# Performance work log

Hardware: AMD Instinct MI355X
Metric: run time of the kernel (lower is better)

The kernel has to match this reference:

```python
import jax, jax.numpy as jnp
import numpy as np

N, E = 50000, 600000
IN, PE, H, L, K = 112, 16, 128, 64, 4


def setup_inputs() -> dict:
    key = jax.random.key(0)
    ks = jax.random.split(key, 8)
    x = jax.random.normal(ks[0], (N, IN), jnp.float32)
    edge_index = jax.random.randint(ks[1], (2, E), 0, N, dtype=jnp.int64)
    lap_pe = jax.random.normal(ks[2], (N, PE), jnp.float32)
    edge_weight = jax.random.uniform(ks[3], (E,), jnp.float32)
    s = lambda k, shp, fan: jax.random.normal(k, shp, jnp.float32) / np.sqrt(fan).astype(np.float32)
    W1 = s(ks[4], (K, IN + PE, H), IN + PE)
    b1 = jnp.zeros((H,), jnp.float32)
    W2 = s(ks[5], (K, H, H), H)
    b2 = jnp.zeros((H,), jnp.float32)
    Wmu = s(ks[6], (H, L), H)
    bmu = jnp.zeros((L,), jnp.float32)
    Wlv = s(ks[7], (H, L), H)
    blv = jnp.zeros((L,), jnp.float32)
    return dict(x=x, edge_index=edge_index, lap_pe=lap_pe, edge_weight=edge_weight,
                W1=W1, b1=b1, W2=W2, b2=b2, Wmu=Wmu, bmu=bmu, Wlv=Wlv, blv=blv)


def _cheb_conv(h, src, dst, w, W, b):
    """PyG ChebConv with precomputed scaled-Laplacian edge weights w.
    T_0 = h ; T_1 = That h ; T_k = 2 That T_{k-1} - T_{k-2}; out = sum_k T_k W_k + b."""
    n = h.shape[0]
    prop = lambda t: jax.ops.segment_sum(w[:, None] * t[src], dst, num_segments=n)
    Tx0 = h
    out = Tx0 @ W[0]
    Tx1 = prop(Tx0)
    out = out + Tx1 @ W[1]
    for k in range(2, W.shape[0]):
        Tx2 = 2.0 * prop(Tx1) - Tx0
        out = out + Tx2 @ W[k]
        Tx0, Tx1 = Tx1, Tx2
    return out + b


def reference(x, edge_index, lap_pe, edge_weight, W1, b1, W2, b2, Wmu, bmu, Wlv, blv):
    n = x.shape[0]
    src, dst = edge_index[0], edge_index[1]
    # sym-normalized Laplacian, lambda_max=2 -> That = L_sym - I = -D^-1/2 A D^-1/2
    deg = jax.ops.segment_sum(edge_weight, src, num_segments=n)
    dis = jnp.where(deg > 0, jax.lax.rsqrt(jnp.maximum(deg, 1e-12)), 0.0)
    w = -dis[src] * edge_weight * dis[dst]
    h = jnp.concatenate([x, lap_pe], axis=1)  # [N, in+pe]
    h = jax.nn.relu(_cheb_conv(h, src, dst, w, W1, b1))
    h = jax.nn.relu(_cheb_conv(h, src, dst, w, W2, b2))
    mu = h @ Wmu + bmu
    logvar = h @ Wlv + blv
    return (mu, logvar)
```

## Files before the change

kernel.cpp:

```cpp
#include <hip/hip_runtime.h>


typedef __bf16 bf16x8 __attribute__((ext_vector_type(8)));
typedef float f32x4 __attribute__((ext_vector_type(4)));
typedef unsigned int uint32;
typedef unsigned short ushort16;

__device__ inline ushort16 f2bf(float f) {
    uint32 x = __float_as_uint(f);
    uint32 r = x + 0x7fffu + ((x >> 16) & 1u);
    return (ushort16)(r >> 16);
}
__device__ inline float bflo(uint32 v) { return __uint_as_float(v << 16); }
__device__ inline float bfhi(uint32 v) { return __uint_as_float(v & 0xffff0000u); }


__global__ void k_deg_cnt(const int* __restrict__ src, const int* __restrict__ dst,
                          const float* __restrict__ ew, float* __restrict__ deg,
                          int* __restrict__ cnt, int* __restrict__ pos,
                          int e0, int e1) {
    int e = e0 + blockIdx.x * blockDim.x + threadIdx.x;
    if (e >= e1) return;
    atomicAdd(&deg[src[e]], ew[e]);
    pos[e] = atomicAdd(&cnt[dst[e]], 1);
}

__global__ void k_scan_blk(const int* __restrict__ cnt, int* __restrict__ row_ptr,
                           int* __restrict__ blk_sums, int N) {
    __shared__ int wsum[4];
    const int tid = threadIdx.x;
    const int base = blockIdx.x * 1024 + tid * 4;
    int4 v = make_int4(0, 0, 0, 0);
    if (base + 3 < N) v = *(const int4*)&cnt[base];
    else {
        if (base + 0 < N) v.x = cnt[base + 0];
        if (base + 1 < N) v.y = cnt[base + 1];
        if (base + 2 < N) v.z = cnt[base + 2];
    }
    const int tsum = v.x + v.y + v.z + v.w;
    const int lane = tid & 63;
    const int wv = tid >> 6;
    int incl = tsum;
    #pragma unroll
    for (int off = 1; off < 64; off <<= 1) {
        int t = __shfl_up(incl, off);
        if (lane >= off) incl += t;
    }
    if (lane == 63) wsum[wv] = incl;
    __syncthreads();
    int woff = 0;
    #pragma unroll
    for (int w = 0; w < 4; ++w) if (w < wv) woff += wsum[w];
    const int excl = woff + incl - tsum;
    if (base + 0 < N) row_ptr[base + 0] = excl;
    if (base + 1 < N) row_ptr[base + 1] = excl + v.x;
    if (base + 2 < N) row_ptr[base + 2] = excl + v.x + v.y;
    if (base + 3 < N) row_ptr[base + 3] = excl + v.x + v.y + v.z;
    if (tid == 255) blk_sums[blockIdx.x] = woff + incl;
}

__global__ void k_scan_top(int* __restrict__ blk_sums, int* __restrict__ row_ptr,
                           int nblk, int N) {
    const int lane = threadIdx.x;
    int v = (lane < nblk) ? blk_sums[lane] : 0;
    int incl = v;
    #pragma unroll
    for (int off = 1; off < 64; off <<= 1) {
        int t = __shfl_up(incl, off);
        if (lane >= off) incl += t;
    }
    if (lane < nblk) blk_sums[lane] = incl - v;
    if (lane == 63) row_ptr[N] = incl;
}

__global__ void k_fix_dis(int* __restrict__ row_ptr, const int* __restrict__ blk_sums,
                          const float* __restrict__ deg, float* __restrict__ dis, int N) {
    int i = blockIdx.x * blockDim.x + threadIdx.x;
    if (i >= N) return;
    row_ptr[i] += blk_sums[i >> 10];
    float d = deg[i];
    dis[i] = d > 0.f ? rsqrtf(fmaxf(d, 1e-12f)) : 0.f;
}

__global__ void k_scatter(const int* __restrict__ src, const int* __restrict__ dst,
                          const float* __restrict__ ew, const float* __restrict__ dis,
                          const int* __restrict__ row_ptr, const int* __restrict__ pos,
                          int2* __restrict__ csr, int E) {
    int e = blockIdx.x * blockDim.x + threadIdx.x;
    if (e >= E) return;
    int s = src[e], d = dst[e];
    float wv = -dis[s] * ew[e] * dis[d];
    csr[row_ptr[d] + pos[e]] = make_int2(s, __float_as_int(wv));
}


__global__ void k_concat_bf16(const float* __restrict__ x, const float* __restrict__ pe,
                              uint32* __restrict__ h, int N) {
    int i4 = (blockIdx.x * blockDim.x + threadIdx.x) * 4;
    if (i4 >= N * 64) return;
    int node = i4 >> 6, p = i4 & 63;
    float4 fa, fb;
    if (p < 56) {
        const float* xp = &x[(size_t)node * 112 + p * 2];
        fa = *(const float4*)xp; fb = *(const float4*)(xp + 4);
    } else {
        const float* pp = &pe[(size_t)node * 16 + (p - 56) * 2];
        fa = *(const float4*)pp; fb = *(const float4*)(pp + 4);
    }
    int4 o;
    o.x = (uint32)f2bf(fa.x) | ((uint32)f2bf(fa.y) << 16);
    o.y = (uint32)f2bf(fa.z) | ((uint32)f2bf(fa.w) << 16);
    o.z = (uint32)f2bf(fb.x) | ((uint32)f2bf(fb.y) << 16);
    o.w = (uint32)f2bf(fb.z) | ((uint32)f2bf(fb.w) << 16);
    *(int4*)&h[i4] = o;
}


__device__ inline float wtrans(const float* __restrict__ W, int kb, size_t o) {
    switch (kb) {
        case 0:  return W[o] - W[o + 32768];
        case 1:  return W[o + 16384] - 3.f * W[o + 49152];
        case 2:  return 2.f * W[o + 32768];
        default: return 4.f * W[o + 49152];
    }
}

__global__ void k_pack_all(const float* __restrict__ W1, const float* __restrict__ W2,
                           const float* __restrict__ Wm, const float* __restrict__ Wl,
                           ushort16* __restrict__ W1p, ushort16* __restrict__ W2p,
                           ushort16* __restrict__ WHp) {
    int t = blockIdx.x * blockDim.x + threadIdx.x;
    uint32 v[8];
    if (t < 16384) {
        const float* W = (t < 8192) ? W1 : W2;
        ushort16* Wp = (t < 8192) ? W1p : W2p;
        int tt = t & 8191;
        int l = tt & 63, c = (tt >> 6) & 7, ks = tt >> 9;
        int kb = ks >> 2;
        int r0 = (ks & 3) * 32 + (l >> 4) * 8;
        int col = c * 16 + (l & 15);
        #pragma unroll
        for (int j = 0; j < 8; ++j)
            v[j] = f2bf(wtrans(W, kb, (size_t)(r0 + j) * 128 + col));
        uint4 o;
        o.x = v[0] | (v[1] << 16); o.y = v[2] | (v[3] << 16);
        o.z = v[4] | (v[5] << 16); o.w = v[6] | (v[7] << 16);
        *(uint4*)(Wp + (size_t)tt * 8) = o;
    } else if (t < 16384 + 2048) {
        int tt = t - 16384;
        int l = tt & 63, c = (tt >> 6) & 7, ks = tt >> 9;
        int k0 = ks * 32 + (l >> 4) * 8;
        int cc = c * 16 + (l & 15);
        const float* Ws = (cc < 64) ? Wm : Wl;
        int col = cc & 63;
        #pragma unroll
        for (int j = 0; j < 8; ++j) v[j] = f2bf(Ws[(size_t)(k0 + j) * 64 + col]);
        uint4 o;
        o.x = v[0] | (v[1] << 16); o.y = v[2] | (v[3] << 16);
        o.z = v[4] | (v[5] << 16); o.w = v[6] | (v[7] << 16);
        *(uint4*)(WHp + (size_t)tt * 8) = o;
    }
}


__global__ void k_prop(const uint32* __restrict__ tin, const int2* __restrict__ csr,
                       const int* __restrict__ row_ptr, uint32* __restrict__ out, int N) {
    int wave = (blockIdx.x * blockDim.x + threadIdx.x) >> 6;
    int lane = threadIdx.x & 63;
    const int half = lane >> 5;
    const int fl = lane & 31;
    int node = wave * 2 + half;
    bool valid = node < N;
    if (!valid) node = N - 1;
    int beg = row_ptr[node];
    int m = valid ? (row_ptr[node + 1] - beg) : 0;
    float a0 = 0.f, a1 = 0.f, a2 = 0.f, a3 = 0.f;
    for (int base = 0; base < m; base += 32) {
        int rem = m - base; if (rem > 32) rem = 32;
        int2 ev = (fl < rem) ? csr[beg + base + fl] : make_int2(0, 0);
        for (int j = 0; j < rem; j += 8) {
            #pragma unroll
            for (int u = 0; u < 8; ++u) {
                int s = __shfl(ev.x, half * 32 + j + u);
                float w = __uint_as_float(__shfl(ev.y, half * 32 + j + u));
                uint2 v = *(const uint2*)&tin[(size_t)s * 64 + fl * 2];
                a0 = fmaf(w, bflo(v.x), a0); a1 = fmaf(w, bfhi(v.x), a1);
                a2 = fmaf(w, bflo(v.y), a2); a3 = fmaf(w, bfhi(v.y), a3);
            }
        }
    }
    if (valid) {
        uint2 o;
        o.x = (uint32)f2bf(a0) | ((uint32)f2bf(a1) << 16);
        o.y = (uint32)f2bf(a2) | ((uint32)f2bf(a3) << 16);
        *(uint2*)&out[(size_t)node * 64 + fl * 2] = o;
    }
}


template<bool RELU>
__launch_bounds__(256)
__global__ void k_mfma_gemm512(const ushort16* __restrict__ t0, const ushort16* __restrict__ t1,
                               const ushort16* __restrict__ t2, const ushort16* __restrict__ t3,
                               const ushort16* __restrict__ Wp, const float* __restrict__ bias,
                               ushort16* __restrict__ C, int N) {
    const int lane = threadIdx.x & 63;
    const int wave = threadIdx.x >> 6;
    const int brow = blockIdx.x * 128 + wave * 32;
    int r0 = brow + (lane & 15);
    int r1 = r0 + 16;
    if (r0 >= N) r0 = N - 1;
    if (r1 >= N) r1 = N - 1;
    const int kg8 = (lane >> 4) * 8;
    f32x4 acc[2][8] = {};
    #pragma unroll
    for (int t = 0; t < 4; ++t) {
        const ushort16* __restrict__ A = (t == 0) ? t0 : (t == 1) ? t1 : (t == 2) ? t2 : t3;
        const ushort16* a0p = A + (size_t)r0 * 128 + kg8;
        const ushort16* a1p = A + (size_t)r1 * 128 + kg8;
        #pragma unroll
        for (int ks2 = 0; ks2 < 4; ++ks2) {
            bf16x8 a0 = *(const bf16x8*)(a0p + ks2 * 32);
            bf16x8 a1 = *(const bf16x8*)(a1p + ks2 * 32);
            const ushort16* bp = Wp + (size_t)((t * 4 + ks2) * 8 * 64 + lane) * 8;
            #pragma unroll
            for (int c = 0; c < 8; ++c) {
                bf16x8 b = *(const bf16x8*)(bp + c * 512);
                acc[0][c] = __builtin_amdgcn_mfma_f32_16x16x32_bf16(a0, b, acc[0][c], 0, 0, 0);
                acc[1][c] = __builtin_amdgcn_mfma_f32_16x16x32_bf16(a1, b, acc[1][c], 0, 0, 0);
            }
        }
    }
    const int col0 = lane & 15;
    const int rj = (lane >> 4) * 4;
    #pragma unroll
    for (int m = 0; m < 2; ++m) {
        #pragma unroll
        for (int c = 0; c < 8; ++c) {
            float bv = bias[c * 16 + col0];
            #pragma unroll
            for (int j = 0; j < 4; ++j) {
                int row = brow + m * 16 + rj + j;
                if (row < N) {
                    float v = acc[m][c][j] + bv;
                    if (RELU) v = fmaxf(v, 0.f);
                    C[(size_t)row * 128 + c * 16 + col0] = f2bf(v);
                }
            }
        }
    }
}


__launch_bounds__(256)
__global__ void k_mfma_head(const ushort16* __restrict__ A, const ushort16* __restrict__ Wp,
                            const float* __restrict__ bm, const float* __restrict__ bl,
                            float* __restrict__ out, int N) {
    const int lane = threadIdx.x & 63;
    const int wave = threadIdx.x >> 6;
    const int brow = blockIdx.x * 128 + wave * 32;
    int r0 = brow + (lane & 15);
    int r1 = r0 + 16;
    if (r0 >= N) r0 = N - 1;
    if (r1 >= N) r1 = N - 1;
    const int kg8 = (lane >> 4) * 8;
    f32x4 acc[2][8] = {};
    const ushort16* a0p = A + (size_t)r0 * 128 + kg8;
    const ushort16* a1p = A + (size_t)r1 * 128 + kg8;
    #pragma unroll
    for (int ks = 0; ks < 4; ++ks) {
        bf16x8 a0 = *(const bf16x8*)(a0p + ks * 32);
        bf16x8 a1 = *(const bf16x8*)(a1p + ks * 32);
        const ushort16* bp = Wp + (size_t)(ks * 8 * 64 + lane) * 8;
        #pragma unroll
        for (int c = 0; c < 8; ++c) {
            bf16x8 b = *(const bf16x8*)(bp + c * 512);
            acc[0][c] = __builtin_amdgcn_mfma_f32_16x16x32_bf16(a0, b, acc[0][c], 0, 0, 0);
            acc[1][c] = __builtin_amdgcn_mfma_f32_16x16x32_bf16(a1, b, acc[1][c], 0, 0, 0);
        }
    }
    const int col0 = lane & 15;
    const int rj = (lane >> 4) * 4;
    #pragma unroll
    for (int m = 0; m < 2; ++m) {
        #pragma unroll
        for (int c = 0; c < 8; ++c) {
            int gcol = (c & 3) * 16 + col0;
            float bv = (c < 4) ? bm[gcol] : bl[gcol];
            size_t hoff = (c < 4) ? 0 : (size_t)N * 64;
            #pragma unroll
            for (int j = 0; j < 4; ++j) {
                int row = brow + m * 16 + rj + j;
                if (row < N)
                    out[hoff + (size_t)row * 64 + gcol] = acc[m][c][j] + bv;
            }
        }
    }
}


extern "C" void kernel_launch(void* const* d_in, const int* in_sizes, int n_in,
                              void* d_out, int out_size, void* d_ws, size_t ws_size,
                              hipStream_t stream) {
    const float* x   = (const float*)d_in[0];
    const int*   ei  = (const int*)d_in[1];
    const float* pe  = (const float*)d_in[2];
    const float* ew  = (const float*)d_in[3];
    const float* W1  = (const float*)d_in[4];
    const float* b1  = (const float*)d_in[5];
    const float* W2  = (const float*)d_in[6];
    const float* b2  = (const float*)d_in[7];
    const float* Wmu = (const float*)d_in[8];
    const float* bmu = (const float*)d_in[9];
    const float* Wlv = (const float*)d_in[10];
    const float* blv = (const float*)d_in[11];

    const int N = in_sizes[0] / 112;
    const int E = in_sizes[1] / 2;
    const int* src = ei;
    const int* dst = ei + E;

    char* ws = (char*)d_ws;
    size_t off = 0;
    auto alloc = [&](size_t bytes) -> char* {
        char* p = ws + off;
        off = (off + bytes + 255) & ~(size_t)255;
        return p;
    };
    float* deg     = (float*)alloc((size_t)N * 4);
    int*   cnt     = (int*)  alloc((size_t)N * 4);
    float* dis     = (float*)alloc((size_t)N * 4);
    int*   row_ptr = (int*)  alloc((size_t)(N + 1) * 4);
    int*   blk_sums= (int*)  alloc((size_t)256 * 4);
    int*   pos     = (int*)  alloc((size_t)E * 4);
    int2*  csr     = (int2*) alloc((size_t)E * 8);
    ushort16* W1p  = (ushort16*)alloc((size_t)512 * 128 * 2);
    ushort16* W2p  = (ushort16*)alloc((size_t)512 * 128 * 2);
    ushort16* WHp  = (ushort16*)alloc((size_t)128 * 128 * 2);
    ushort16* B0 = (ushort16*)alloc((size_t)N * 128 * 2);
    ushort16* B1 = (ushort16*)alloc((size_t)N * 128 * 2);
    ushort16* B2 = (ushort16*)alloc((size_t)N * 128 * 2);
    ushort16* B3 = (ushort16*)alloc((size_t)N * 128 * 2);
    ushort16* B4 = (ushort16*)alloc((size_t)N * 128 * 2);

    hipMemsetAsync(deg, 0, (size_t)N * 4, stream);
    hipMemsetAsync(cnt, 0, (size_t)N * 4, stream);

    const int eb4 = (E / 4 + 255) / 256;
    const int nb = (N + 255) / 256;
    const int pb = ((N + 1) / 2 + 3) / 4;
    const int gb = (N + 127) / 128;
    const int nblk = (N + 1023) / 1024;
    const int cb = (N * 64 + 1023) / 1024;

    for (int q = 0; q < 4; ++q) {
        int e0 = (int)((size_t)E * q / 4);
        int e1 = (int)((size_t)E * (q + 1) / 4);
        k_deg_cnt<<<eb4, 256, 0, stream>>>(src, dst, ew, deg, cnt, pos, e0, e1);
    }
    k_scan_blk<<<nblk, 256, 0, stream>>>(cnt, row_ptr, blk_sums, N);
    k_scan_top<<<1, 64, 0, stream>>>(blk_sums, row_ptr, nblk, N);
    k_fix_dis<<<nb, 256, 0, stream>>>(row_ptr, blk_sums, deg, dis, N);
    k_scatter<<<(E + 255) / 256, 256, 0, stream>>>(src, dst, ew, dis, row_ptr, pos, csr, E);
    k_concat_bf16<<<cb, 256, 0, stream>>>(x, pe, (uint32*)B0, N);
    k_pack_all<<<(16384 + 2048 + 255) / 256, 256, 0, stream>>>(W1, W2, Wmu, Wlv, W1p, W2p, WHp);

    k_prop<<<pb, 256, 0, stream>>>((uint32*)B0, csr, row_ptr, (uint32*)B1, N);
    k_prop<<<pb, 256, 0, stream>>>((uint32*)B1, csr, row_ptr, (uint32*)B2, N);
    k_prop<<<pb, 256, 0, stream>>>((uint32*)B2, csr, row_ptr, (uint32*)B3, N);
    k_mfma_gemm512<true><<<gb, 256, 0, stream>>>(B0, B1, B2, B3, W1p, b1, B4, N);

    k_prop<<<pb, 256, 0, stream>>>((uint32*)B4, csr, row_ptr, (uint32*)B0, N);
    k_prop<<<pb, 256, 0, stream>>>((uint32*)B0, csr, row_ptr, (uint32*)B1, N);
    k_prop<<<pb, 256, 0, stream>>>((uint32*)B1, csr, row_ptr, (uint32*)B2, N);
    k_mfma_gemm512<true><<<gb, 256, 0, stream>>>(B4, B0, B1, B2, W2p, b2, B3, N);

    k_mfma_head<<<gb, 256, 0, stream>>>(B3, WHp, bmu, blv, (float*)d_out, N);
}
```

Measured before the change: 312.0 us.

## Fuse second Cheb GEMM with head, single-block scan, one-wave-per-node propagation

Three separate changes. The second-layer GEMM and the mu/logvar head are fused into one kernel that stages the ReLU'd hidden tile in swizzled LDS, so the N×128 intermediate no longer goes to and from global memory. The three-kernel multi-block scan is replaced by a single 1024-thread block scan plus a separate dis kernel, which cuts launches but serialises the scan onto one CU. The propagation kernel switches from two nodes per wave with 8-byte gathers to one node per wave with 4-byte gathers per lane, trading edge-level parallelism for different memory access granularity.

```diff
diff --git a/kernel.cpp b/kernel.cpp
--- a/kernel.cpp
+++ b/kernel.cpp
@@ -25,59 +25,41 @@
     pos[e] = atomicAdd(&cnt[dst[e]], 1);
 }
 
-__global__ void k_scan_blk(const int* __restrict__ cnt, int* __restrict__ row_ptr,
-                           int* __restrict__ blk_sums, int N) {
-    __shared__ int wsum[4];
-    const int tid = threadIdx.x;
-    const int base = blockIdx.x * 1024 + tid * 4;
-    int4 v = make_int4(0, 0, 0, 0);
-    if (base + 3 < N) v = *(const int4*)&cnt[base];
-    else {
-        if (base + 0 < N) v.x = cnt[base + 0];
-        if (base + 1 < N) v.y = cnt[base + 1];
-        if (base + 2 < N) v.z = cnt[base + 2];
-    }
-    const int tsum = v.x + v.y + v.z + v.w;
-    const int lane = tid & 63;
-    const int wv = tid >> 6;
-    int incl = tsum;
+__launch_bounds__(1024)
+__global__ void k_scan_one(const int* __restrict__ cnt, int* __restrict__ row_ptr, int N) {
+    __shared__ int wsum[16];
+    const int t = threadIdx.x;
+    const int C = (N + 1023) / 1024;
+    const int base = t * C;
+    int s = 0;
+    for (int i = 0; i < C; ++i) {
+        int idx = base + i;
+        if (idx < N) s += cnt[idx];
+    }
+    const int lane = t & 63;
+    const int wv = t >> 6;
+    int incl = s;
     #pragma unroll
     for (int off = 1; off < 64; off <<= 1) {
-        int t = __shfl_up(incl, off);
-        if (lane >= off) incl += t;
+        int u = __shfl_up(incl, off);
+        if (lane >= off) incl += u;
     }
     if (lane == 63) wsum[wv] = incl;
     __syncthreads();
     int woff = 0;
     #pragma unroll
-    for (int w = 0; w < 4; ++w) if (w < wv) woff += wsum[w];
-    const int excl = woff + incl - tsum;
-    if (base + 0 < N) row_ptr[base + 0] = excl;
-    if (base + 1 < N) row_ptr[base + 1] = excl + v.x;
-    if (base + 2 < N) row_ptr[base + 2] = excl + v.x + v.y;
-    if (base + 3 < N) row_ptr[base + 3] = excl + v.x + v.y + v.z;
-    if (tid == 255) blk_sums[blockIdx.x] = woff + incl;
-}
-
-__global__ void k_scan_top(int* __restrict__ blk_sums, int* __restrict__ row_ptr,
-                           int nblk, int N) {
-    const int lane = threadIdx.x;
-    int v = (lane < nblk) ? blk_sums[lane] : 0;
-    int incl = v;
-    #pragma unroll
-    for (int off = 1; off < 64; off <<= 1) {
-        int t = __shfl_up(incl, off);
-        if (lane >= off) incl += t;
-    }
-    if (lane < nblk) blk_sums[lane] = incl - v;
-    if (lane == 63) row_ptr[N] = incl;
-}
-
-__global__ void k_fix_dis(int* __restrict__ row_ptr, const int* __restrict__ blk_sums,
-                          const float* __restrict__ deg, float* __restrict__ dis, int N) {
+    for (int w = 0; w < 16; ++w) if (w < wv) woff += wsum[w];
+    int run = woff + incl - s;
+    for (int i = 0; i < C; ++i) {
+        int idx = base + i;
+        if (idx < N) { row_ptr[idx] = run; run += cnt[idx]; }
+    }
+    if (t == 1023) row_ptr[N] = run;
+}
+
+__global__ void k_dis(const float* __restrict__ deg, float* __restrict__ dis, int N) {
     int i = blockIdx.x * blockDim.x + threadIdx.x;
     if (i >= N) return;
-    row_ptr[i] += blk_sums[i >> 10];
     float d = deg[i];
     dis[i] = d > 0.f ? rsqrtf(fmaxf(d, 1e-12f)) : 0.f;
 }
@@ -165,36 +147,25 @@
 
 __global__ void k_prop(const uint32* __restrict__ tin, const int2* __restrict__ csr,
                        const int* __restrict__ row_ptr, uint32* __restrict__ out, int N) {
-    int wave = (blockIdx.x * blockDim.x + threadIdx.x) >> 6;
+    int wid = (blockIdx.x * blockDim.x + threadIdx.x) >> 6;
     int lane = threadIdx.x & 63;
-    const int half = lane >> 5;
-    const int fl = lane & 31;
-    int node = wave * 2 + half;
-    bool valid = node < N;
-    if (!valid) node = N - 1;
-    int beg = row_ptr[node];
-    int m = valid ? (row_ptr[node + 1] - beg) : 0;
-    float a0 = 0.f, a1 = 0.f, a2 = 0.f, a3 = 0.f;
-    for (int base = 0; base < m; base += 32) {
-        int rem = m - base; if (rem > 32) rem = 32;
-        int2 ev = (fl < rem) ? csr[beg + base + fl] : make_int2(0, 0);
-        for (int j = 0; j < rem; j += 8) {
+    if (wid >= N) return;
+    int beg = row_ptr[wid], end = row_ptr[wid + 1];
+    float ax = 0.f, ay = 0.f;
+    for (int base = beg; base < end; base += 64) {
+        int m = end - base; if (m > 64) m = 64;
+        int2 ev = (lane < m) ? csr[base + lane] : make_int2(0, 0);
+        for (int j = 0; j < m; j += 8) {
             #pragma unroll
             for (int u = 0; u < 8; ++u) {
-                int s = __shfl(ev.x, half * 32 + j + u);
-                float w = __uint_as_float(__shfl(ev.y, half * 32 + j + u));
-                uint2 v = *(const uint2*)&tin[(size_t)s * 64 + fl * 2];
-                a0 = fmaf(w, bflo(v.x), a0); a1 = fmaf(w, bfhi(v.x), a1);
-                a2 = fmaf(w, bflo(v.y), a2); a3 = fmaf(w, bfhi(v.y), a3);
-            }
-        }
-    }
-    if (valid) {
-        uint2 o;
-        o.x = (uint32)f2bf(a0) | ((uint32)f2bf(a1) << 16);
-        o.y = (uint32)f2bf(a2) | ((uint32)f2bf(a3) << 16);
-        *(uint2*)&out[(size_t)node * 64 + fl * 2] = o;
-    }
+                int s = __shfl(ev.x, j + u);
+                float w = __uint_as_float(__shfl(ev.y, j + u));
+                uint32 v = tin[(size_t)s * 64 + lane];
+                ax = fmaf(w, bflo(v), ax); ay = fmaf(w, bfhi(v), ay);
+            }
+        }
+    }
+    out[(size_t)wid * 64 + lane] = (uint32)f2bf(ax) | ((uint32)f2bf(ay) << 16);
 }
 
 
@@ -253,9 +224,12 @@
 
 
 __launch_bounds__(256)
-__global__ void k_mfma_head(const ushort16* __restrict__ A, const ushort16* __restrict__ Wp,
-                            const float* __restrict__ bm, const float* __restrict__ bl,
-                            float* __restrict__ out, int N) {
+__global__ void k_gemm2_head(const ushort16* __restrict__ t0, const ushort16* __restrict__ t1,
+                             const ushort16* __restrict__ t2, const ushort16* __restrict__ t3,
+                             const ushort16* __restrict__ Wp, const float* __restrict__ bias,
+                             const ushort16* __restrict__ WHp, const float* __restrict__ bm,
+                             const float* __restrict__ bl, float* __restrict__ out, int N) {
+    __shared__ ushort16 lds_c[128 * 128];
     const int lane = threadIdx.x & 63;
     const int wave = threadIdx.x >> 6;
     const int brow = blockIdx.x * 128 + wave * 32;
@@ -264,23 +238,60 @@
     if (r0 >= N) r0 = N - 1;
     if (r1 >= N) r1 = N - 1;
     const int kg8 = (lane >> 4) * 8;
+    const int col0 = lane & 15;
+    const int rj = (lane >> 4) * 4;
+
     f32x4 acc[2][8] = {};
-    const ushort16* a0p = A + (size_t)r0 * 128 + kg8;
-    const ushort16* a1p = A + (size_t)r1 * 128 + kg8;
+    #pragma unroll
+    for (int t = 0; t < 4; ++t) {
+        const ushort16* __restrict__ A = (t == 0) ? t0 : (t == 1) ? t1 : (t == 2) ? t2 : t3;
+        const ushort16* a0p = A + (size_t)r0 * 128 + kg8;
+        const ushort16* a1p = A + (size_t)r1 * 128 + kg8;
+        #pragma unroll
+        for (int ks2 = 0; ks2 < 4; ++ks2) {
+            bf16x8 a0 = *(const bf16x8*)(a0p + ks2 * 32);
+            bf16x8 a1 = *(const bf16x8*)(a1p + ks2 * 32);
+            const ushort16* bp = Wp + (size_t)((t * 4 + ks2) * 8 * 64 + lane) * 8;
+            #pragma unroll
+            for (int c = 0; c < 8; ++c) {
+                bf16x8 b = *(const bf16x8*)(bp + c * 512);
+                acc[0][c] = __builtin_amdgcn_mfma_f32_16x16x32_bf16(a0, b, acc[0][c], 0, 0, 0);
+                acc[1][c] = __builtin_amdgcn_mfma_f32_16x16x32_bf16(a1, b, acc[1][c], 0, 0, 0);
+            }
+        }
+    }
+    #pragma unroll
+    for (int m = 0; m < 2; ++m) {
+        #pragma unroll
+        for (int c = 0; c < 8; ++c) {
+            float bv = bias[c * 16 + col0];
+            #pragma unroll
+            for (int j = 0; j < 4; ++j) {
+                int lr = wave * 32 + m * 16 + rj + j;
+                float v = fmaxf(acc[m][c][j] + bv, 0.f);
+                int col = c * 16 + col0;
+                lds_c[lr * 128 + (col ^ ((lr & 7) << 3))] = f2bf(v);
+            }
+        }
+    }
+    __syncthreads();
+
+    const int lr0 = wave * 32 + (lane & 15);
+    const int lr1 = lr0 + 16;
+    f32x4 acc2[2][8] = {};
     #pragma unroll
     for (int ks = 0; ks < 4; ++ks) {
-        bf16x8 a0 = *(const bf16x8*)(a0p + ks * 32);
-        bf16x8 a1 = *(const bf16x8*)(a1p + ks * 32);
-        const ushort16* bp = Wp + (size_t)(ks * 8 * 64 + lane) * 8;
+        int h = ks * 32 + kg8;
+        bf16x8 a0 = *(const bf16x8*)&lds_c[lr0 * 128 + (h ^ ((lr0 & 7) << 3))];
+        bf16x8 a1 = *(const bf16x8*)&lds_c[lr1 * 128 + (h ^ ((lr1 & 7) << 3))];
+        const ushort16* bp = WHp + (size_t)(ks * 8 * 64 + lane) * 8;
         #pragma unroll
         for (int c = 0; c < 8; ++c) {
             bf16x8 b = *(const bf16x8*)(bp + c * 512);
-            acc[0][c] = __builtin_amdgcn_mfma_f32_16x16x32_bf16(a0, b, acc[0][c], 0, 0, 0);
-            acc[1][c] = __builtin_amdgcn_mfma_f32_16x16x32_bf16(a1, b, acc[1][c], 0, 0, 0);
-        }
-    }
-    const int col0 = lane & 15;
-    const int rj = (lane >> 4) * 4;
+            acc2[0][c] = __builtin_amdgcn_mfma_f32_16x16x32_bf16(a0, b, acc2[0][c], 0, 0, 0);
+            acc2[1][c] = __builtin_amdgcn_mfma_f32_16x16x32_bf16(a1, b, acc2[1][c], 0, 0, 0);
+        }
+    }
     #pragma unroll
     for (int m = 0; m < 2; ++m) {
         #pragma unroll
@@ -292,7 +303,7 @@
             for (int j = 0; j < 4; ++j) {
                 int row = brow + m * 16 + rj + j;
                 if (row < N)
-                    out[hoff + (size_t)row * 64 + gcol] = acc[m][c][j] + bv;
+                    out[hoff + (size_t)row * 64 + gcol] = acc2[m][c][j] + bv;
             }
         }
     }
@@ -331,7 +342,6 @@
     int*   cnt     = (int*)  alloc((size_t)N * 4);
     float* dis     = (float*)alloc((size_t)N * 4);
     int*   row_ptr = (int*)  alloc((size_t)(N + 1) * 4);
-    int*   blk_sums= (int*)  alloc((size_t)256 * 4);
     int*   pos     = (int*)  alloc((size_t)E * 4);
     int2*  csr     = (int2*) alloc((size_t)E * 8);
     ushort16* W1p  = (ushort16*)alloc((size_t)512 * 128 * 2);
@@ -348,9 +358,8 @@
 
     const int eb4 = (E / 4 + 255) / 256;
     const int nb = (N + 255) / 256;
-    const int pb = ((N + 1) / 2 + 3) / 4;
+    const int pb = (N + 3) / 4;
     const int gb = (N + 127) / 128;
-    const int nblk = (N + 1023) / 1024;
     const int cb = (N * 64 + 1023) / 1024;
 
     for (int q = 0; q < 4; ++q) {
@@ -358,9 +367,8 @@
         int e1 = (int)((size_t)E * (q + 1) / 4);
         k_deg_cnt<<<eb4, 256, 0, stream>>>(src, dst, ew, deg, cnt, pos, e0, e1);
     }
-    k_scan_blk<<<nblk, 256, 0, stream>>>(cnt, row_ptr, blk_sums, N);
-    k_scan_top<<<1, 64, 0, stream>>>(blk_sums, row_ptr, nblk, N);
-    k_fix_dis<<<nb, 256, 0, stream>>>(row_ptr, blk_sums, deg, dis, N);
+    k_scan_one<<<1, 1024, 0, stream>>>(cnt, row_ptr, N);
+    k_dis<<<nb, 256, 0, stream>>>(deg, dis, N);
     k_scatter<<<(E + 255) / 256, 256, 0, stream>>>(src, dst, ew, dis, row_ptr, pos, csr, E);
     k_concat_bf16<<<cb, 256, 0, stream>>>(x, pe, (uint32*)B0, N);
     k_pack_all<<<(16384 + 2048 + 255) / 256, 256, 0, stream>>>(W1, W2, Wmu, Wlv, W1p, W2p, WHp);
@@ -373,7 +381,6 @@
     k_prop<<<pb, 256, 0, stream>>>((uint32*)B4, csr, row_ptr, (uint32*)B0, N);
     k_prop<<<pb, 256, 0, stream>>>((uint32*)B0, csr, row_ptr, (uint32*)B1, N);
     k_prop<<<pb, 256, 0, stream>>>((uint32*)B1, csr, row_ptr, (uint32*)B2, N);
-    k_mfma_gemm512<true><<<gb, 256, 0, stream>>>(B4, B0, B1, B2, W2p, b2, B3, N);
-
-    k_mfma_head<<<gb, 256, 0, stream>>>(B3, WHp, bmu, blv, (float*)d_out, N);
-}
+    k_gemm2_head<<<gb, 256, 0, stream>>>(B4, B0, B1, B2, W2p, b2, WHp, bmu, blv,
+                                         (float*)d_out, N);
+}
```

Result: slower. 412.6 us (+32.2%).
